# Kernel tuning notes

Measured on AMD Instinct MI355X. Metric: run time of the kernel, lower is better.

The kernel has to match this reference:

```python
import jax, jax.numpy as jnp
import numpy as np

B, C, H, W = 4, 64, 128, 128
NUM_HEAD = 1
SCALE = (C // NUM_HEAD) ** (-0.5)


def setup_inputs():
    key = jax.random.key(0)
    ks = jax.random.split(key, 32)
    def nrm(k, shape, s=0.05):
        return jax.random.normal(k, shape, jnp.float32) * s
    inp = {"x": jax.random.normal(ks[0], (B, C, H, W), jnp.float32)}
    i = 1
    for wn, bn in [("Wq", "bq"), ("Wk", "bk"), ("Wv", "bv"), ("Wl", "bl"), ("Wo", "bo"), ("Wp", "bp")]:
        inp[wn] = nrm(ks[i], (C, C)); i += 1
        inp[bn] = nrm(ks[i], (C,)); i += 1
    inp["sch_dw"] = nrm(ks[i], (C, 1, 5, 1)); i += 1
    inp["sch_dwb"] = nrm(ks[i], (C,)); i += 1
    inp["sch_pw"] = nrm(ks[i], (C, C, 1, 1)); i += 1
    inp["sch_pwb"] = nrm(ks[i], (C,)); i += 1
    inp["scv_dw"] = nrm(ks[i], (C, 1, 1, 5)); i += 1
    inp["scv_dwb"] = nrm(ks[i], (C,)); i += 1
    inp["scv_pw"] = nrm(ks[i], (C, C, 1, 1)); i += 1
    inp["scv_pwb"] = nrm(ks[i], (C,)); i += 1
    inp["convh_w"] = nrm(ks[i], (C, C, 1, 1)); i += 1
    inp["convh_b"] = nrm(ks[i], (C,)); i += 1
    inp["dsc_dw"] = nrm(ks[i], (C, 1, 3, 3)); i += 1
    inp["dsc_dwb"] = nrm(ks[i], (C,)); i += 1
    inp["dsc_pw"] = nrm(ks[i], (C, C, 1, 1)); i += 1
    inp["dsc_pwb"] = nrm(ks[i], (C,)); i += 1
    inp["ln_g"] = jnp.ones((C,), jnp.float32)
    inp["ln_b"] = jnp.zeros((C,), jnp.float32)
    return inp


def _linear(x, w, b):  # x [B,N,C], w [C,C] (torch Linear convention: y = x @ w.T + b)
    return x @ w.T + b


def _dwconv(x, w, b, pad):  # depthwise: x [B,C,H,W], w [C,1,kh,kw]
    y = jax.lax.conv_general_dilated(x, w, (1, 1), [(pad[0], pad[0]), (pad[1], pad[1])],
                                     dimension_numbers=("NCHW", "OIHW", "NCHW"),
                                     feature_group_count=x.shape[1])
    return y + b[None, :, None, None]


def _pwconv(x, w, b):  # 1x1 conv: w [Co,Ci,1,1]
    return jnp.einsum("bchw,oc->bohw", x, w[:, :, 0, 0]) + b[None, :, None, None]


def _attn(q, k, v):  # [B,N,C] each; dense NxN softmax attention
    a = jax.nn.softmax(jnp.einsum("bnc,bmc->bnm", q, k) * SCALE, axis=-1)
    return jnp.einsum("bnm,bmc->bnc", a, v)


def _up2_bilinear(x):  # bilinear, scale 2, align_corners=True
    Bb, Cc, Hh, Ww = x.shape
    def coords(n):
        s = jnp.linspace(0.0, n - 1.0, 2 * n)
        i0 = jnp.floor(s).astype(jnp.int32)
        i1 = jnp.minimum(i0 + 1, n - 1)
        return i0, i1, (s - i0).astype(x.dtype)
    y0, y1, wy = coords(Hh)
    x0, x1, wx = coords(Ww)
    r = x[:, :, y0, :] * (1.0 - wy)[None, None, :, None] + x[:, :, y1, :] * wy[None, None, :, None]
    return r[:, :, :, x0] * (1.0 - wx) + r[:, :, :, x1] * wx


def _forward(x, Wq, bq, Wk, bk, Wv, bv, Wl, bl, Wo, bo, Wp, bp,
             sch_dw, sch_dwb, sch_pw, sch_pwb, scv_dw, scv_dwb, scv_pw, scv_pwb,
             convh_w, convh_b, dsc_dw, dsc_dwb, dsc_pw, dsc_pwb, ln_g, ln_b):
    Bb, Cc, Hh, Ww = x.shape
    # AvgPool2d(2,2)
    xp = x.reshape(Bb, Cc, Hh // 2, 2, Ww // 2, 2).mean((3, 5))
    Hp, Wp_ = Hh // 2, Ww // 2
    N = Hp * Wp_
    # forward_lpg: GAP-gated self-attention producing low-freq prompt
    gap = xp.mean((2, 3), keepdims=True)
    xg = (gap * xp).reshape(Bb, Cc, N).transpose(0, 2, 1)  # [B,N,C]
    q = _linear(xg, Wq, bq); k = _linear(xg, Wk, bk); v = _linear(xg, Wv, bv)
    prompt_l = _linear(_attn(q, k, v), Wl, bl).transpose(0, 2, 1).reshape(Bb, Cc, Hp, Wp_)
    # forward_hpg: separable strip-conv branches -> high-freq prompt
    x_h = _pwconv(jax.nn.gelu(_dwconv(xp, sch_dw, sch_dwb, (2, 0)), approximate=False), sch_pw, sch_pwb)
    x_v = _pwconv(jax.nn.gelu(_dwconv(xp, scv_dw, scv_dwb, (0, 2)), approximate=False), scv_pw, scv_pwb)
    prompt_h = _pwconv(x_h + x_v, convh_w, convh_b)
    # forward_pgc: cross-attention Q=high, K=low, V=linear(x)
    x_V = _linear(xp.reshape(Bb, Cc, N).transpose(0, 2, 1), Wo, bo)
    x_K = prompt_l.reshape(Bb, Cc, N).transpose(0, 2, 1)
    x_Q = prompt_h.reshape(Bb, Cc, N).transpose(0, 2, 1)
    prompt = _attn(x_Q, x_K, x_V)
    prompt = _linear(prompt, Wp, bp) + x_V
    # LayerNorm over channel dim
    mu = prompt.mean(-1, keepdims=True)
    var = jnp.mean((prompt - mu) ** 2, axis=-1, keepdims=True)
    p_norm = (prompt - mu) / jnp.sqrt(var + 1e-5) * ln_g + ln_b
    p_norm = p_norm.transpose(0, 2, 1).reshape(Bb, Cc, Hp, Wp_)
    # dsc: depthwise 3x3 -> GELU -> 1x1, residual
    out = _pwconv(jax.nn.gelu(_dwconv(p_norm, dsc_dw, dsc_dwb, (1, 1)), approximate=False), dsc_pw, dsc_pwb) + p_norm
    return _up2_bilinear(out)


def reference(x, Wq, bq, Wk, bk, Wv, bv, Wl, bl, Wo, bo, Wp, bp,
              sch_dw, sch_dwb, sch_pw, sch_pwb, scv_dw, scv_dwb, scv_pw, scv_pwb,
              convh_w, convh_b, dsc_dw, dsc_dwb, dsc_pw, dsc_pwb, ln_g, ln_b):
    return _forward(x, Wq, bq, Wk, bk, Wv, bv, Wl, bl, Wo, bo, Wp, bp,
                    sch_dw, sch_dwb, sch_pw, sch_pwb, scv_dw, scv_dwb, scv_pw, scv_pwb,
                    convh_w, convh_b, dsc_dw, dsc_dwb, dsc_pw, dsc_pwb, ln_g, ln_b)
```

## Files before the change

### kernel.cpp

```cpp
#include <hip/hip_runtime.h>
#include <math.h>

#define Bn 4
#define Cn 64
#define Np 4096
#define NSPLIT 4
#define SCALE2 0.18033688011112042f

typedef unsigned short ushort_t;
typedef __attribute__((ext_vector_type(4))) float f32x4;
typedef __attribute__((ext_vector_type(8))) short bf16x8;
typedef __attribute__((ext_vector_type(4))) short bf16x4;

__device__ __forceinline__ float gelu_exact(float x) {
    return 0.5f * x * (1.0f + erff(x * 0.70710678118654752440f));
}
__device__ __forceinline__ ushort_t f2bf(float f) {
    unsigned int u = __float_as_uint(f);
    u += 0x7fffu + ((u >> 16) & 1u);
    return (ushort_t)(u >> 16);
}
__device__ __forceinline__ ushort_t f2bf_tr(float f) {
    return (ushort_t)(__float_as_uint(f) >> 16);
}
__device__ __forceinline__ float bf2f(ushort_t h) {
    return __uint_as_float(((unsigned int)h) << 16);
}
__device__ __forceinline__ void gload_lds16(const ushort_t* g, ushort_t* l) {
    __builtin_amdgcn_global_load_lds(
        (const __attribute__((address_space(1))) void*)g,
        (__attribute__((address_space(3))) void*)l, 16, 0, 0);
}
__device__ __forceinline__ bf16x8 cvt8(const float v[8]) {
    bf16x8 r;
    #pragma unroll
    for (int j = 0; j < 8; ++j) r[j] = (short)f2bf(v[j]);
    return r;
}
__device__ __forceinline__ void gemm16b(const bf16x8 af[2], const ushort_t* __restrict__ Wb,
                                        int l16, int quad, f32x4* acc) {
    #pragma unroll
    for (int cb = 0; cb < 4; ++cb) {
        #pragma unroll
        for (int ks = 0; ks < 2; ++ks) {
            bf16x8 bw = *(const bf16x8*)(Wb + (cb * 16 + l16) * 64 + ks * 32 + quad * 8);
            acc[cb] = __builtin_amdgcn_mfma_f32_16x16x32_bf16(af[ks], bw, acc[cb], 0, 0, 0);
        }
    }
}
__device__ __forceinline__ void gemm16Tb(const bf16x8 af[2], const ushort_t* __restrict__ Wb,
                                         int l16, int quad, f32x4* acc) {
    #pragma unroll
    for (int cb = 0; cb < 4; ++cb) {
        #pragma unroll
        for (int ks = 0; ks < 2; ++ks) {
            bf16x8 bw = *(const bf16x8*)(Wb + (cb * 16 + l16) * 64 + ks * 32 + quad * 8);
            acc[cb] = __builtin_amdgcn_mfma_f32_16x16x32_bf16(bw, af[ks], acc[cb], 0, 0, 0);
        }
    }
}
__device__ __forceinline__ void aload(const float* xs, int row, int quad, bf16x8 af[2]) {
    #pragma unroll
    for (int ks = 0; ks < 2; ++ks) {
        float v[8];
        #pragma unroll
        for (int j = 0; j < 8; ++j) v[j] = xs[(ks * 32 + quad * 8 + j) * 65 + row];
        af[ks] = cvt8(v);
    }
}
__device__ __forceinline__ void stage_bchw(const float* __restrict__ X, int b, int n0, int t,
                                           float* xs) {
    #pragma unroll
    for (int u = 0; u < 16; ++u) {
        int idx = t + u * 256;
        int c = idx >> 6, nl = idx & 63;
        xs[c * 65 + nl] = X[((size_t)(b * Cn + c)) * Np + n0 + nl];
    }
}
__device__ __forceinline__ void stage_comb(const ushort_t* __restrict__ OpB, const float* linv,
                                           int b, int n0, int t, float* xs) {
    const size_t SS = (size_t)Bn * Np * Cn;
    int c4 = (t & 15) * 4;
    #pragma unroll
    for (int u = 0; u < 4; ++u) {
        int nl = (t >> 4) + u * 16;
        size_t gi = ((size_t)(b * Np + n0 + nl)) * Cn + c4;
        ushort4 a0 = *(const ushort4*)(OpB + gi);
        ushort4 a1 = *(const ushort4*)(OpB + SS + gi);
        ushort4 a2 = *(const ushort4*)(OpB + 2 * SS + gi);
        ushort4 a3 = *(const ushort4*)(OpB + 3 * SS + gi);
        float li = linv[nl];
        xs[(c4 + 0) * 65 + nl] = (bf2f(a0.x) + bf2f(a1.x) + bf2f(a2.x) + bf2f(a3.x)) * li;
        xs[(c4 + 1) * 65 + nl] = (bf2f(a0.y) + bf2f(a1.y) + bf2f(a2.y) + bf2f(a3.y)) * li;
        xs[(c4 + 2) * 65 + nl] = (bf2f(a0.z) + bf2f(a1.z) + bf2f(a2.z) + bf2f(a3.z)) * li;
        xs[(c4 + 3) * 65 + nl] = (bf2f(a0.w) + bf2f(a1.w) + bf2f(a2.w) + bf2f(a3.w)) * li;
    }
}
__device__ __forceinline__ void store_bnc_T(ushort_t* __restrict__ Y, int b, int n, int quad,
                                            const f32x4* acc, const float* __restrict__ bias,
                                            float mult) {
    #pragma unroll
    for (int cb = 0; cb < 4; ++cb) {
        int o0 = cb * 16 + quad * 4;
        ushort4 pk;
        pk.x = f2bf((acc[cb][0] + bias[o0 + 0]) * mult);
        pk.y = f2bf((acc[cb][1] + bias[o0 + 1]) * mult);
        pk.z = f2bf((acc[cb][2] + bias[o0 + 2]) * mult);
        pk.w = f2bf((acc[cb][3] + bias[o0 + 3]) * mult);
        *(ushort4*)(Y + ((size_t)(b * Np + n)) * Cn + o0) = pk;
    }
}
__device__ __forceinline__ void store_bchw_bf16(ushort_t* __restrict__ Y, int b, int nb, int l16,
                                                const f32x4* acc, const float* __restrict__ bias) {
    #pragma unroll
    for (int cb = 0; cb < 4; ++cb) {
        int col = cb * 16 + l16;
        float bb = bias[col];
        ushort4 pk;
        pk.x = f2bf(acc[cb][0] + bb); pk.y = f2bf(acc[cb][1] + bb);
        pk.z = f2bf(acc[cb][2] + bb); pk.w = f2bf(acc[cb][3] + bb);
        *(ushort4*)(Y + ((size_t)(b * Cn + col)) * Np + nb) = pk;
    }
}

__global__ void avgpool_kernel(const float* __restrict__ x, float* __restrict__ xp,
                               float* __restrict__ gap4k,
                               const float* __restrict__ convh_w, const float* __restrict__ convh_b,
                               const float* __restrict__ sch_pw, const float* __restrict__ sch_pwb,
                               const float* __restrict__ scv_pw, const float* __restrict__ scv_pwb,
                               ushort_t* __restrict__ Wc1b, ushort_t* __restrict__ Wc2b,
                               float* __restrict__ bcv,
                               const float* __restrict__ Wq, const float* __restrict__ Wk,
                               const float* __restrict__ Wv, const float* __restrict__ Wo,
                               const float* __restrict__ Wl, const float* __restrict__ Wp,
                               const float* __restrict__ dscpw, ushort_t* __restrict__ Wball) {
    if (blockIdx.x < 4096) {
        int idx = blockIdx.x * 256 + threadIdx.x;
        int j  = idx & 63;
        int i  = (idx >> 6) & 63;
        int bc = idx >> 12;
        const float* p = x + ((size_t)bc * 128 + 2 * i) * 128 + 2 * j;
        float v = 0.25f * (p[0] + p[1] + p[128] + p[129]);
        xp[idx] = v;
        float s = v;
        #pragma unroll
        for (int off = 1; off < 64; off <<= 1) s += __shfl_xor(s, off, 64);
        __shared__ float sm[4];
        if ((threadIdx.x & 63) == 0) sm[threadIdx.x >> 6] = s;
        __syncthreads();
        if (threadIdx.x == 0) gap4k[blockIdx.x] = sm[0] + sm[1] + sm[2] + sm[3];
    } else if (blockIdx.x < 4128) {
        int g = (blockIdx.x - 4096) * 256 + threadIdx.x;
        int sel = g >> 12, idx = g & 4095;
        int o = idx >> 6, c = idx & 63;
        const float* pw = sel ? scv_pw : sch_pw;
        float acc = 0.f;
        #pragma unroll 8
        for (int m = 0; m < 64; ++m) acc += convh_w[o * 64 + m] * pw[m * 64 + c];
        (sel ? Wc2b : Wc1b)[idx] = f2bf(acc * SCALE2);
        if (g < 64) {
            float ab = convh_b[g];
            for (int m = 0; m < 64; ++m) ab += convh_w[g * 64 + m] * (sch_pwb[m] + scv_pwb[m]);
            bcv[g] = ab * SCALE2;
        }
    } else {
        int g = (blockIdx.x - 4128) * 256 + threadIdx.x;
        int which = g >> 12, idx = g & 4095;
        const float* srcs[7] = {Wq, Wk, Wv, Wo, Wl, Wp, dscpw};
        Wball[g] = f2bf(srcs[which][idx]);
    }
}

__global__ __launch_bounds__(256) void qkv_dw_kernel(
    const float* __restrict__ xp, const float* __restrict__ gap4k,
    const ushort_t* __restrict__ Wqb, const float* __restrict__ bq,
    const ushort_t* __restrict__ Wkb, const float* __restrict__ bk,
    const ushort_t* __restrict__ Wvb, const float* __restrict__ bv,
    const ushort_t* __restrict__ Wob, const float* __restrict__ bo,
    ushort_t* __restrict__ qb, ushort_t* __restrict__ kb, ushort_t* __restrict__ vb,
    float* __restrict__ xV, ushort_t* __restrict__ xVtb,
    const float* __restrict__ wv5, const float* __restrict__ bv5,
    const float* __restrict__ wh5, const float* __restrict__ bh5,
    ushort_t* __restrict__ gh, ushort_t* __restrict__ gv) {
    int b = blockIdx.y, t = threadIdx.x;
    if (blockIdx.x >= 64) {
        int part = blockIdx.x - 64;
        int e = part * 1024 + t * 4;
        size_t base = (size_t)b * (Cn * Np) + e;
        int c = e >> 12, i = (e >> 6) & 63, j = e & 63;
        const float* p = xp + ((size_t)(b * Cn + c)) * Np;
        float accV[4], accH[4];
        #pragma unroll
        for (int k = 0; k < 4; ++k) { accV[k] = bv5[c]; accH[k] = bh5[c]; }
        #pragma unroll
        for (int d = 0; d < 5; ++d) {
            int ii = i + d - 2;
            if (ii >= 0 && ii < 64) {
                f32x4 r = *(const f32x4*)(p + ii * 64 + j);
                float w = wv5[c * 5 + d];
                accV[0] += w * r[0]; accV[1] += w * r[1];
                accV[2] += w * r[2]; accV[3] += w * r[3];
            }
        }
        f32x4 c0 = *(const f32x4*)(p + i * 64 + j);
        float col[8];
        col[2] = c0[0]; col[3] = c0[1]; col[4] = c0[2]; col[5] = c0[3];
        col[0] = (j >= 2)     ? p[i * 64 + j - 2] : 0.f;
        col[1] = (j >= 1)     ? p[i * 64 + j - 1] : 0.f;
        col[6] = (j + 4 < 64) ? p[i * 64 + j + 4] : 0.f;
        col[7] = (j + 5 < 64) ? p[i * 64 + j + 5] : 0.f;
        #pragma unroll
        for (int k = 0; k < 4; ++k) {
            #pragma unroll
            for (int d = 0; d < 5; ++d) accH[k] += wh5[c * 5 + d] * col[k + d];
        }
        ushort4 ph, pv_;
        ph.x = f2bf(gelu_exact(accV[0])); ph.y = f2bf(gelu_exact(accV[1]));
        ph.z = f2bf(gelu_exact(accV[2])); ph.w = f2bf(gelu_exact(accV[3]));
        pv_.x = f2bf(gelu_exact(accH[0])); pv_.y = f2bf(gelu_exact(accH[1]));
        pv_.z = f2bf(gelu_exact(accH[2])); pv_.w = f2bf(gelu_exact(accH[3]));
        *(ushort4*)(gh + base) = ph;
        *(ushort4*)(gv + base) = pv_;
        return;
    }
    __shared__ float xs[64 * 65];
    __shared__ float gl[64];
    int n0 = blockIdx.x * 64;
    int wv_ = t >> 6, lane = t & 63, l16 = lane & 15, quad = lane >> 4;
    stage_bchw(xp, b, n0, t, xs);
    if (t < 64) {
        float s = 0.f;
        #pragma unroll
        for (int u = 0; u < 16; ++u) s += gap4k[(b * 64 + t) * 16 + u];
        gl[t] = s * (1.f / 4096.f);
    }
    __syncthreads();
    int row = wv_ * 16 + l16;
    int n   = n0 + wv_ * 16 + l16;
    int nb  = n0 + wv_ * 16 + quad * 4;
    bf16x8 ar[2], ag[2];
    #pragma unroll
    for (int ks = 0; ks < 2; ++ks) {
        float vr[8], vg[8];
        #pragma unroll
        for (int j = 0; j < 8; ++j) {
            int k = ks * 32 + quad * 8 + j;
            float xv = xs[k * 65 + row];
            vr[j] = xv; vg[j] = xv * gl[k];
        }
        ar[ks] = cvt8(vr); ag[ks] = cvt8(vg);
    }
    f32x4 acc[4];
    #pragma unroll
    for (int cb = 0; cb < 4; ++cb) acc[cb] = (f32x4){0.f, 0.f, 0.f, 0.f};
    gemm16Tb(ag, Wqb, l16, quad, acc);
    store_bnc_T(qb, b, n, quad, acc, bq, SCALE2);
    #pragma unroll
    for (int cb = 0; cb < 4; ++cb) acc[cb] = (f32x4){0.f, 0.f, 0.f, 0.f};
    gemm16Tb(ag, Wkb, l16, quad, acc);
    store_bnc_T(kb, b, n, quad, acc, bk, 1.f);
    #pragma unroll
    for (int cb = 0; cb < 4; ++cb) acc[cb] = (f32x4){0.f, 0.f, 0.f, 0.f};
    gemm16b(ag, Wvb, l16, quad, acc);
    store_bchw_bf16(vb, b, nb, l16, acc, bv);
    #pragma unroll
    for (int cb = 0; cb < 4; ++cb) acc[cb] = (f32x4){0.f, 0.f, 0.f, 0.f};
    gemm16b(ar, Wob, l16, quad, acc);
    #pragma unroll
    for (int cb = 0; cb < 4; ++cb) {
        int col = cb * 16 + l16;
        float bb = bo[col];
        ushort4 pk;
        float y0 = acc[cb][0] + bb, y1 = acc[cb][1] + bb, y2 = acc[cb][2] + bb, y3 = acc[cb][3] + bb;
        xV[((size_t)(b * Np + nb + 0)) * Cn + col] = y0;
        xV[((size_t)(b * Np + nb + 1)) * Cn + col] = y1;
        xV[((size_t)(b * Np + nb + 2)) * Cn + col] = y2;
        xV[((size_t)(b * Np + nb + 3)) * Cn + col] = y3;
        pk.x = f2bf(y0); pk.y = f2bf(y1); pk.z = f2bf(y2); pk.w = f2bf(y3);
        *(ushort4*)(xVtb + ((size_t)(b * Cn + col)) * Np + nb) = pk;
    }
}

__device__ __forceinline__ void attn_wave(
    int wid, int b, const ushort_t* __restrict__ Qb, const ushort_t* __restrict__ Kb,
    const ushort_t* __restrict__ Vtb, ushort_t* __restrict__ OpB, float* __restrict__ Lpart,
    ushort_t* lds ) {
    int split = wid >> 7;
    int qt    = wid & 127;
    int n0    = qt * 32;
    int lane  = threadIdx.x & 63;
    int l16   = lane & 15, quad = lane >> 4;
    int kvbase = split * (Np / NSPLIT);

    const ushort_t* qp = Qb + ((size_t)(b * Np) + n0 + l16) * Cn + quad * 8;
    bf16x8 aq00 = *(const bf16x8*)(qp);
    bf16x8 aq01 = *(const bf16x8*)(qp + 32);
    bf16x8 aq10 = *(const bf16x8*)(qp + 16 * Cn);
    bf16x8 aq11 = *(const bf16x8*)(qp + 16 * Cn + 32);
    asm volatile("s_waitcnt vmcnt(0)" ::: "memory");

    f32x4 oa0[4], oa1[4];
    float psum0 = 0.f, psum1 = 0.f;
    #pragma unroll
    for (int db = 0; db < 4; ++db) {
        oa0[db] = (f32x4){0.f, 0.f, 0.f, 0.f};
        oa1[db] = (f32x4){0.f, 0.f, 0.f, 0.f};
    }

    const ushort_t* gK = Kb + ((size_t)b * Np + kvbase + (lane >> 3)) * Cn
                            + (((lane & 7) ^ (lane >> 3)) * 8);
    const ushort_t* gV = Vtb + ((size_t)(b * Cn) + (lane >> 1)) * Np + kvbase + (lane & 1) * 8;
    ushort_t* kl = lds;
    ushort_t* vl = lds + 2048;

    const ushort_t* kr0 = lds + l16 * 64 + ((quad      ^ (l16 & 7))) * 8;
    const ushort_t* kr1 = lds + l16 * 64 + (((quad + 4) ^ (l16 & 7))) * 8;
    const ushort_t* vrb = lds + 2048 + l16 * 16 + quad * 4;

    auto stage = [&](int buf) {
        ushort_t* kd = kl + buf * 1024;
        gload_lds16(gK,       kd);
        gload_lds16(gK + 512, kd + 512);
        ushort_t* vd = vl + buf * 1024;
        gload_lds16(gV,                   vd);
        gload_lds16(gV + (size_t)32 * Np, vd + 512);
        gK += 16 * Cn;
        gV += 16;
    };

    auto compute = [&](int ko) {
        bf16x8 k0 = *(const bf16x8*)(kr0 + ko);
        bf16x8 k1 = *(const bf16x8*)(kr1 + ko);
        f32x4 sa0 = (f32x4){0.f, 0.f, 0.f, 0.f};
        f32x4 sa1 = (f32x4){0.f, 0.f, 0.f, 0.f};
        __builtin_amdgcn_s_setprio(1);
        sa0 = __builtin_amdgcn_mfma_f32_16x16x32_bf16(k0, aq00, sa0, 0, 0, 0);
        sa0 = __builtin_amdgcn_mfma_f32_16x16x32_bf16(k1, aq01, sa0, 0, 0, 0);
        sa1 = __builtin_amdgcn_mfma_f32_16x16x32_bf16(k0, aq10, sa1, 0, 0, 0);
        sa1 = __builtin_amdgcn_mfma_f32_16x16x32_bf16(k1, aq11, sa1, 0, 0, 0);
        __builtin_amdgcn_s_setprio(0);
        float p0 = exp2f(sa0[0]), p1 = exp2f(sa0[1]), p2 = exp2f(sa0[2]), p3 = exp2f(sa0[3]);
        psum0 += (p0 + p1) + (p2 + p3);
        bf16x4 pb0;
        pb0[0] = (short)f2bf_tr(p0); pb0[1] = (short)f2bf_tr(p1);
        pb0[2] = (short)f2bf_tr(p2); pb0[3] = (short)f2bf_tr(p3);
        float q0 = exp2f(sa1[0]), q1 = exp2f(sa1[1]), q2 = exp2f(sa1[2]), q3 = exp2f(sa1[3]);
        psum1 += (q0 + q1) + (q2 + q3);
        bf16x4 pb1;
        pb1[0] = (short)f2bf_tr(q0); pb1[1] = (short)f2bf_tr(q1);
        pb1[2] = (short)f2bf_tr(q2); pb1[3] = (short)f2bf_tr(q3);
        __builtin_amdgcn_s_setprio(1);
        #pragma unroll
        for (int db = 0; db < 4; ++db) {
            bf16x4 av = *(const bf16x4*)(vrb + ko + db * 256);
            oa0[db] = __builtin_amdgcn_mfma_f32_16x16x16bf16_1k(av, pb0, oa0[db], 0, 0, 0);
            oa1[db] = __builtin_amdgcn_mfma_f32_16x16x16bf16_1k(av, pb1, oa1[db], 0, 0, 0);
        }
        __builtin_amdgcn_s_setprio(0);
    };

    const int NT = (Np / NSPLIT) / 16;
    stage(0);
    #pragma unroll 1
    for (int mm = 0; mm < NT / 2; ++mm) {
        stage(1);
        asm volatile("s_waitcnt vmcnt(4)" ::: "memory");
        compute(0);
        if (mm < NT / 2 - 1) {
            stage(0);
            asm volatile("s_waitcnt vmcnt(4)" ::: "memory");
        } else {
            asm volatile("s_waitcnt vmcnt(0)" ::: "memory");
        }
        compute(1024);
    }

    psum0 += __shfl_xor(psum0, 16, 64);
    psum0 += __shfl_xor(psum0, 32, 64);
    psum1 += __shfl_xor(psum1, 16, 64);
    psum1 += __shfl_xor(psum1, 32, 64);
    size_t obase = ((size_t)(split * Bn + b)) * Np;
    int n = n0 + l16;
    if (quad == 0) {
        Lpart[obase + n]      = psum0;
        Lpart[obase + n + 16] = psum1;
    }
    #pragma unroll
    for (int db = 0; db < 4; ++db) {
        ushort4 pk;
        pk.x = f2bf(oa0[db][0]); pk.y = f2bf(oa0[db][1]);
        pk.z = f2bf(oa0[db][2]); pk.w = f2bf(oa0[db][3]);
        *(ushort4*)(OpB + (obase + n) * Cn + db * 16 + quad * 4) = pk;
        ushort4 qk;
        qk.x = f2bf(oa1[db][0]); qk.y = f2bf(oa1[db][1]);
        qk.z = f2bf(oa1[db][2]); qk.w = f2bf(oa1[db][3]);
        *(ushort4*)(OpB + (obase + n + 16) * Cn + db * 16 + quad * 4) = qk;
    }
}

__device__ __forceinline__ void hpg_body(
    int tile, int b, const ushort_t* __restrict__ gh, const ushort_t* __restrict__ gv,
    const ushort_t* __restrict__ Wc1b, const ushort_t* __restrict__ Wc2b,
    const float* __restrict__ bcv,
    ushort_t* __restrict__ xQb, ushort_t* smem) {
    ushort_t* xs1 = smem;
    ushort_t* xs2 = smem + 4608;
    int n0 = tile * 64, t = threadIdx.x;
    int wv_ = t >> 6, lane = t & 63, l16 = lane & 15, quad = lane >> 4;
    #pragma unroll
    for (int u = 0; u < 4; ++u) {
        int lin = u * 256 + t;
        int c = lin >> 4, nl4 = (lin & 15) * 4;
        size_t gi = ((size_t)(b * Cn + c)) * Np + n0 + nl4;
        ushort4 g1 = *(const ushort4*)(gh + gi);
        ushort4 g2 = *(const ushort4*)(gv + gi);
        xs1[(nl4 + 0) * 72 + c] = g1.x; xs1[(nl4 + 1) * 72 + c] = g1.y;
        xs1[(nl4 + 2) * 72 + c] = g1.z; xs1[(nl4 + 3) * 72 + c] = g1.w;
        xs2[(nl4 + 0) * 72 + c] = g2.x; xs2[(nl4 + 1) * 72 + c] = g2.y;
        xs2[(nl4 + 2) * 72 + c] = g2.z; xs2[(nl4 + 3) * 72 + c] = g2.w;
    }
    __syncthreads();
    int row = wv_ * 16 + l16;
    bf16x8 a1[2], a2[2];
    #pragma unroll
    for (int ks = 0; ks < 2; ++ks) {
        a1[ks] = *(const bf16x8*)(xs1 + row * 72 + ks * 32 + quad * 8);
        a2[ks] = *(const bf16x8*)(xs2 + row * 72 + ks * 32 + quad * 8);
    }
    f32x4 acc[4];
    #pragma unroll
    for (int cb = 0; cb < 4; ++cb) acc[cb] = (f32x4){0.f, 0.f, 0.f, 0.f};
    gemm16Tb(a1, Wc1b, l16, quad, acc);
    gemm16Tb(a2, Wc2b, l16, quad, acc);
    store_bnc_T(xQb, b, n0 + wv_ * 16 + l16, quad, acc, bcv, 1.f);
}

__global__ __launch_bounds__(256) void attn_hpg_kernel(
    const ushort_t* __restrict__ Qb, const ushort_t* __restrict__ Kb,
    const ushort_t* __restrict__ Vtb, ushort_t* __restrict__ OpB, float* __restrict__ Lpart,
    const ushort_t* __restrict__ gh, const ushort_t* __restrict__ gv,
    const ushort_t* __restrict__ Wc1b, const ushort_t* __restrict__ Wc2b,
    const float* __restrict__ bcv, ushort_t* __restrict__ xQb) {
    __shared__ ushort_t smem[16384];
    int b = blockIdx.y;
    if (blockIdx.x < 128) {
        int wave = threadIdx.x >> 6;
        attn_wave(blockIdx.x * 4 + wave, b, Qb, Kb, Vtb, OpB, Lpart, smem + wave * 4096);
    } else {
        hpg_body(blockIdx.x - 128, b, gh, gv, Wc1b, Wc2b, bcv, xQb, smem);
    }
}

__global__ __launch_bounds__(256) void wl_mfma(
    const ushort_t* __restrict__ OpB, const float* __restrict__ Lp,
    const ushort_t* __restrict__ Wlb, const float* __restrict__ bl, ushort_t* __restrict__ xKb) {
    __shared__ float xs[64 * 65];
    __shared__ float linv[64];
    int b = blockIdx.y, n0 = blockIdx.x * 64, t = threadIdx.x;
    int wv_ = t >> 6, lane = t & 63, l16 = lane & 15, quad = lane >> 4;
    if (t < 64) {
        size_t li = (size_t)b * Np + n0 + t;
        const size_t LS = (size_t)Bn * Np;
        linv[t] = 1.f / (Lp[li] + Lp[LS + li] + Lp[2 * LS + li] + Lp[3 * LS + li]);
    }
    __syncthreads();
    stage_comb(OpB, linv, b, n0, t, xs);
    __syncthreads();
    bf16x8 af[2];
    aload(xs, wv_ * 16 + l16, quad, af);
    f32x4 acc[4];
    #pragma unroll
    for (int cb = 0; cb < 4; ++cb) acc[cb] = (f32x4){0.f, 0.f, 0.f, 0.f};
    gemm16Tb(af, Wlb, l16, quad, acc);
    store_bnc_T(xKb, b, n0 + wv_ * 16 + l16, quad, acc, bl, 1.f);
}

__global__ __launch_bounds__(256) void linln_mfma(
    const ushort_t* __restrict__ OpB, const float* __restrict__ Lp,
    const ushort_t* __restrict__ Wpb, const float* __restrict__ bp,
    const float* __restrict__ xV, const float* __restrict__ g, const float* __restrict__ beta,
    float* __restrict__ out) {
    __shared__ float xs[64 * 65];
    __shared__ float linv[64];
    int b = blockIdx.y, n0 = blockIdx.x * 64, t = threadIdx.x;
    int wv_ = t >> 6, lane = t & 63, l16 = lane & 15, quad = lane >> 4;
    if (t < 64) {
        size_t li = (size_t)b * Np + n0 + t;
        const size_t LS = (size_t)Bn * Np;
        linv[t] = 1.f / (Lp[li] + Lp[LS + li] + Lp[2 * LS + li] + Lp[3 * LS + li]);
    }
    __syncthreads();
    stage_comb(OpB, linv, b, n0, t, xs);
    __syncthreads();
    bf16x8 af[2];
    aload(xs, wv_ * 16 + l16, quad, af);
    f32x4 acc[4];
    #pragma unroll
    for (int cb = 0; cb < 4; ++cb) acc[cb] = (f32x4){0.f, 0.f, 0.f, 0.f};
    gemm16b(af, Wpb, l16, quad, acc);
    int nb = n0 + wv_ * 16 + quad * 4;
    float vals[4][4], gc[4], bec[4];
    #pragma unroll
    for (int cb = 0; cb < 4; ++cb) {
        int col = cb * 16 + l16;
        float bb = bp[col];
        gc[cb] = g[col]; bec[cb] = beta[col];
        #pragma unroll
        for (int r = 0; r < 4; ++r)
            vals[cb][r] = acc[cb][r] + bb + xV[((size_t)(b * Np + nb + r)) * Cn + col];
    }
    f32x4 yn[4];
    #pragma unroll
    for (int r = 0; r < 4; ++r) {
        float s = 0.f, s2 = 0.f;
        #pragma unroll
        for (int cb = 0; cb < 4; ++cb) { s += vals[cb][r]; s2 += vals[cb][r] * vals[cb][r]; }
        #pragma unroll
        for (int off = 1; off < 16; off <<= 1) {
            s  += __shfl_xor(s, off, 64);
            s2 += __shfl_xor(s2, off, 64);
        }
        float mu  = s * (1.f / 64.f);
        float var = s2 * (1.f / 64.f) - mu * mu;
        float ivs = rsqrtf(var + 1e-5f);
        #pragma unroll
        for (int cb = 0; cb < 4; ++cb)
            yn[cb][r] = (vals[cb][r] - mu) * ivs * gc[cb] + bec[cb];
    }
    #pragma unroll
    for (int cb = 0; cb < 4; ++cb)
        *(f32x4*)(out + ((size_t)(b * Cn + cb * 16 + l16)) * Np + nb) = yn[cb];
}

__global__ __launch_bounds__(256) void dsc_mfma(
    const float* __restrict__ X, const float* __restrict__ dw, const float* __restrict__ dwb,
    const ushort_t* __restrict__ Wb, const float* __restrict__ bias, float* __restrict__ out) {
    __shared__ float xs[64 * 65];
    int b = blockIdx.y, irow = blockIdx.x, n0 = irow * 64, t = threadIdx.x;
    int wv_ = t >> 6, lane = t & 63, l16 = lane & 15, quad = lane >> 4;
    int j = t & 63;
    #pragma unroll
    for (int u = 0; u < 16; ++u) {
        int c = (t >> 6) + u * 4;
        const float* p = X + ((size_t)(b * Cn + c)) * Np + n0;
        float acc = dwb[c];
        #pragma unroll
        for (int dy = 0; dy < 3; ++dy) {
            int ii = irow + dy - 1;
            if (ii < 0 || ii >= 64) continue;
            const float* pr = p + (dy - 1) * 64;
            #pragma unroll
            for (int dx = 0; dx < 3; ++dx) {
                int jj = j + dx - 1;
                if (jj < 0 || jj >= 64) continue;
                acc += dw[c * 9 + dy * 3 + dx] * pr[jj];
            }
        }
        xs[c * 65 + j] = gelu_exact(acc);
    }
    __syncthreads();
    bf16x8 af[2];
    aload(xs, wv_ * 16 + l16, quad, af);
    f32x4 acc[4];
    #pragma unroll
    for (int cb = 0; cb < 4; ++cb) acc[cb] = (f32x4){0.f, 0.f, 0.f, 0.f};
    gemm16b(af, Wb, l16, quad, acc);
    int nb = n0 + wv_ * 16 + quad * 4;
    #pragma unroll
    for (int cb = 0; cb < 4; ++cb) {
        int col = cb * 16 + l16;
        float bb = bias[col];
        size_t oi = ((size_t)(b * Cn + col)) * Np + nb;
        f32x4 rv = *(const f32x4*)(X + oi);
        f32x4 v4;
        #pragma unroll
        for (int r = 0; r < 4; ++r) v4[r] = acc[cb][r] + bb + rv[r];
        *(f32x4*)(out + oi) = v4;
    }
}

__global__ void upsample_kernel(const float* __restrict__ in, float* __restrict__ out) {
    int idx = blockIdx.x * 256 + threadIdx.x;
    int x4 = (idx & 31) * 4;
    int y  = (idx >> 5) & 127;
    int bc = idx >> 12;
    float sy = y * (63.f / 127.f);
    int y0 = (int)sy;
    float fy = sy - y0;
    int y1 = min(y0 + 1, 63);
    const float* p0 = in + (size_t)bc * Np + y0 * 64;
    const float* p1 = in + (size_t)bc * Np + y1 * 64;
    f32x4 o;
    #pragma unroll
    for (int k = 0; k < 4; ++k) {
        int xo = x4 + k;
        float sx = xo * (63.f / 127.f);
        int x0 = (int)sx;
        float fx = sx - x0;
        int x1 = min(x0 + 1, 63);
        float r0 = p0[x0] + (p0[x1] - p0[x0]) * fx;
        float r1 = p1[x0] + (p1[x1] - p1[x0]) * fx;
        o[k] = r0 + (r1 - r0) * fy;
    }
    *(f32x4*)(out + (size_t)idx * 4) = o;
}

extern "C" void kernel_launch(void* const* d_in, const int* in_sizes, int n_in,
                              void* d_out, int out_size, void* d_ws, size_t ws_size,
                              hipStream_t stream) {
    const float* x       = (const float*)d_in[0];
    const float* Wq      = (const float*)d_in[1];
    const float* bq      = (const float*)d_in[2];
    const float* Wk      = (const float*)d_in[3];
    const float* bk      = (const float*)d_in[4];
    const float* Wv      = (const float*)d_in[5];
    const float* bv      = (const float*)d_in[6];
    const float* Wl      = (const float*)d_in[7];
    const float* bl      = (const float*)d_in[8];
    const float* Wo      = (const float*)d_in[9];
    const float* bo      = (const float*)d_in[10];
    const float* Wp      = (const float*)d_in[11];
    const float* bp      = (const float*)d_in[12];
    const float* sch_dw  = (const float*)d_in[13];
    const float* sch_dwb = (const float*)d_in[14];
    const float* sch_pw  = (const float*)d_in[15];
    const float* sch_pwb = (const float*)d_in[16];
    const float* scv_dw  = (const float*)d_in[17];
    const float* scv_dwb = (const float*)d_in[18];
    const float* scv_pw  = (const float*)d_in[19];
    const float* scv_pwb = (const float*)d_in[20];
    const float* convh_w = (const float*)d_in[21];
    const float* convh_b = (const float*)d_in[22];
    const float* dsc_dw  = (const float*)d_in[23];
    const float* dsc_dwb = (const float*)d_in[24];
    const float* dsc_pw  = (const float*)d_in[25];
    const float* dsc_pwb = (const float*)d_in[26];
    const float* ln_g    = (const float*)d_in[27];
    const float* ln_b    = (const float*)d_in[28];

    float* ws = (float*)d_ws;
    const size_t SZ = (size_t)Bn * Np * Cn;
    float* xp   = ws;
    float* xV   = ws + SZ;
    ushort_t* ghb = (ushort_t*)(ws + 2 * SZ);
    ushort_t* gh  = ghb;
    ushort_t* gv  = ghb + SZ;
    float* f2   = ws + 2 * SZ;
    ushort_t* bws  = (ushort_t*)(ws + 3 * SZ);
    ushort_t* qb   = bws;
    ushort_t* kb_  = bws + SZ;
    ushort_t* vb   = bws + 2 * SZ;
    ushort_t* xKb  = bws + 3 * SZ;
    ushort_t* xVtb = bws + 4 * SZ;
    ushort_t* xQb  = bws + 5 * SZ;
    ushort_t* OpB  = (ushort_t*)(ws + 6 * SZ);
    float* gap4k  = ws + 8 * SZ;
    float* Lpart  = gap4k + 4096;
    float* wcslot = Lpart + (size_t)NSPLIT * Bn * Np;
    ushort_t* Wc1b = (ushort_t*)wcslot;
    ushort_t* Wc2b = Wc1b + 4096;
    float* bcv  = wcslot + 4096;
    ushort_t* Wball = (ushort_t*)(bcv + 64);
    ushort_t* Wqb   = Wball;
    ushort_t* Wkb   = Wball + 4096;
    ushort_t* Wvb   = Wball + 8192;
    ushort_t* Wob   = Wball + 12288;
    ushort_t* Wlb   = Wball + 16384;
    ushort_t* Wpb   = Wball + 20480;
    ushort_t* Wdscb = Wball + 24576;

    dim3 g64(64, Bn);

    avgpool_kernel<<<4096 + 32 + 112, 256, 0, stream>>>(x, xp, gap4k,
                                                  convh_w, convh_b, sch_pw, sch_pwb,
                                                  scv_pw, scv_pwb, Wc1b, Wc2b, bcv,
                                                  Wq, Wk, Wv, Wo, Wl, Wp, dsc_pw, Wball);
    qkv_dw_kernel<<<dim3(64 + 256, Bn), 256, 0, stream>>>(
        xp, gap4k, Wqb, bq, Wkb, bk, Wvb, bv, Wob, bo,
        qb, kb_, vb, xV, xVtb, sch_dw, sch_dwb, scv_dw, scv_dwb, gh, gv);
    attn_hpg_kernel<<<dim3(128 + 64, Bn), 256, 0, stream>>>(
        qb, kb_, vb, OpB, Lpart, gh, gv, Wc1b, Wc2b, bcv, xQb);
    wl_mfma<<<g64, 256, 0, stream>>>(OpB, Lpart, Wlb, bl, xKb);
    attn_hpg_kernel<<<dim3(128, Bn), 256, 0, stream>>>(
        xQb, xKb, xVtb, OpB, Lpart, gh, gv, Wc1b, Wc2b, bcv, xQb);
    linln_mfma<<<g64, 256, 0, stream>>>(OpB, Lpart, Wpb, bp, xV, ln_g, ln_b, xp);
    dsc_mfma<<<g64, 256, 0, stream>>>(xp, dsc_dw, dsc_dwb, Wdscb, dsc_pwb, f2);
    upsample_kernel<<<4096, 256, 0, stream>>>(f2, (float*)d_out);
}
```

Baseline: 267.0 us.

## Double KV split count in attention and swizzle V tile in LDS

Raises the flash-attention KV split factor from 4 to 8, doubling the attention grid to 1024 blocks so more of the GPU's compute units are occupied. The combine step in the Wl and LN kernels now loops over all partials, and the workspace layout is shifted to make room for the larger partial-output buffer. Separately, the V tile's LDS layout gets an XOR swizzle on its 8-element halves to reduce bank conflicts on reads. The cost is twice the partial-output traffic written and then reduced by the combine kernels.

```diff
diff --git a/kernel.cpp b/kernel.cpp
--- a/kernel.cpp
+++ b/kernel.cpp
@@ -4,7 +4,7 @@
 #define Bn 4
 #define Cn 64
 #define Np 4096
-#define NSPLIT 4
+#define NSPLIT 8
 #define SCALE2 0.18033688011112042f
 
 typedef unsigned short ushort_t;
@@ -85,15 +85,17 @@
     for (int u = 0; u < 4; ++u) {
         int nl = (t >> 4) + u * 16;
         size_t gi = ((size_t)(b * Np + n0 + nl)) * Cn + c4;
-        ushort4 a0 = *(const ushort4*)(OpB + gi);
-        ushort4 a1 = *(const ushort4*)(OpB + SS + gi);
-        ushort4 a2 = *(const ushort4*)(OpB + 2 * SS + gi);
-        ushort4 a3 = *(const ushort4*)(OpB + 3 * SS + gi);
+        float s0 = 0.f, s1 = 0.f, s2 = 0.f, s3 = 0.f;
+        #pragma unroll
+        for (int sp = 0; sp < NSPLIT; ++sp) {
+            ushort4 a = *(const ushort4*)(OpB + (size_t)sp * SS + gi);
+            s0 += bf2f(a.x); s1 += bf2f(a.y); s2 += bf2f(a.z); s3 += bf2f(a.w);
+        }
         float li = linv[nl];
-        xs[(c4 + 0) * 65 + nl] = (bf2f(a0.x) + bf2f(a1.x) + bf2f(a2.x) + bf2f(a3.x)) * li;
-        xs[(c4 + 1) * 65 + nl] = (bf2f(a0.y) + bf2f(a1.y) + bf2f(a2.y) + bf2f(a3.y)) * li;
-        xs[(c4 + 2) * 65 + nl] = (bf2f(a0.z) + bf2f(a1.z) + bf2f(a2.z) + bf2f(a3.z)) * li;
-        xs[(c4 + 3) * 65 + nl] = (bf2f(a0.w) + bf2f(a1.w) + bf2f(a2.w) + bf2f(a3.w)) * li;
+        xs[(c4 + 0) * 65 + nl] = s0 * li;
+        xs[(c4 + 1) * 65 + nl] = s1 * li;
+        xs[(c4 + 2) * 65 + nl] = s2 * li;
+        xs[(c4 + 3) * 65 + nl] = s3 * li;
     }
 }
 __device__ __forceinline__ void store_bnc_T(ushort_t* __restrict__ Y, int b, int n, int quad,
@@ -309,13 +311,15 @@
 
     const ushort_t* gK = Kb + ((size_t)b * Np + kvbase + (lane >> 3)) * Cn
                             + (((lane & 7) ^ (lane >> 3)) * 8);
-    const ushort_t* gV = Vtb + ((size_t)(b * Cn) + (lane >> 1)) * Np + kvbase + (lane & 1) * 8;
+    const ushort_t* gV = Vtb + ((size_t)(b * Cn) + (lane >> 1)) * Np + kvbase
+                             + (((lane & 1) ^ ((lane >> 3) & 1)) * 8);
     ushort_t* kl = lds;
     ushort_t* vl = lds + 2048;
 
     const ushort_t* kr0 = lds + l16 * 64 + ((quad      ^ (l16 & 7))) * 8;
     const ushort_t* kr1 = lds + l16 * 64 + (((quad + 4) ^ (l16 & 7))) * 8;
-    const ushort_t* vrb = lds + 2048 + l16 * 16 + quad * 4;
+    const ushort_t* vrb = lds + 2048 + l16 * 16
+                        + (((quad >> 1) ^ ((l16 >> 2) & 1)) * 8) + (quad & 1) * 4;
 
     auto stage = [&](int buf) {
         ushort_t* kd = kl + buf * 1024;
@@ -443,11 +447,11 @@
     const float* __restrict__ bcv, ushort_t* __restrict__ xQb) {
     __shared__ ushort_t smem[16384];
     int b = blockIdx.y;
-    if (blockIdx.x < 128) {
+    if (blockIdx.x < 256) {
         int wave = threadIdx.x >> 6;
         attn_wave(blockIdx.x * 4 + wave, b, Qb, Kb, Vtb, OpB, Lpart, smem + wave * 4096);
     } else {
-        hpg_body(blockIdx.x - 128, b, gh, gv, Wc1b, Wc2b, bcv, xQb, smem);
+        hpg_body(blockIdx.x - 256, b, gh, gv, Wc1b, Wc2b, bcv, xQb, smem);
     }
 }
 
@@ -461,7 +465,10 @@
     if (t < 64) {
         size_t li = (size_t)b * Np + n0 + t;
         const size_t LS = (size_t)Bn * Np;
-        linv[t] = 1.f / (Lp[li] + Lp[LS + li] + Lp[2 * LS + li] + Lp[3 * LS + li]);
+        float s = 0.f;
+        #pragma unroll
+        for (int sp = 0; sp < NSPLIT; ++sp) s += Lp[(size_t)sp * LS + li];
+        linv[t] = 1.f / s;
     }
     __syncthreads();
     stage_comb(OpB, linv, b, n0, t, xs);
@@ -487,7 +494,10 @@
     if (t < 64) {
         size_t li = (size_t)b * Np + n0 + t;
         const size_t LS = (size_t)Bn * Np;
-        linv[t] = 1.f / (Lp[li] + Lp[LS + li] + Lp[2 * LS + li] + Lp[3 * LS + li]);
+        float s = 0.f;
+        #pragma unroll
+        for (int sp = 0; sp < NSPLIT; ++sp) s += Lp[(size_t)sp * LS + li];
+        linv[t] = 1.f / s;
     }
     __syncthreads();
     stage_comb(OpB, linv, b, n0, t, xs);
@@ -654,7 +664,7 @@
     ushort_t* xVtb = bws + 4 * SZ;
     ushort_t* xQb  = bws + 5 * SZ;
     ushort_t* OpB  = (ushort_t*)(ws + 6 * SZ);
-    float* gap4k  = ws + 8 * SZ;
+    float* gap4k  = ws + 10 * SZ;
     float* Lpart  = gap4k + 4096;
     float* wcslot = Lpart + (size_t)NSPLIT * Bn * Np;
     ushort_t* Wc1b = (ushort_t*)wcslot;
@@ -678,10 +688,10 @@
     qkv_dw_kernel<<<dim3(64 + 256, Bn), 256, 0, stream>>>(
         xp, gap4k, Wqb, bq, Wkb, bk, Wvb, bv, Wob, bo,
         qb, kb_, vb, xV, xVtb, sch_dw, sch_dwb, scv_dw, scv_dwb, gh, gv);
-    attn_hpg_kernel<<<dim3(128 + 64, Bn), 256, 0, stream>>>(
+    attn_hpg_kernel<<<dim3(256 + 64, Bn), 256, 0, stream>>>(
         qb, kb_, vb, OpB, Lpart, gh, gv, Wc1b, Wc2b, bcv, xQb);
     wl_mfma<<<g64, 256, 0, stream>>>(OpB, Lpart, Wlb, bl, xKb);
-    attn_hpg_kernel<<<dim3(128, Bn), 256, 0, stream>>>(
+    attn_hpg_kernel<<<dim3(256, Bn), 256, 0, stream>>>(
         xQb, xKb, xVtb, OpB, Lpart, gh, gv, Wc1b, Wc2b, bcv, xQb);
     linln_mfma<<<g64, 256, 0, stream>>>(OpB, Lpart, Wpb, bp, xV, ln_g, ln_b, xp);
     dsc_mfma<<<g64, 256, 0, stream>>>(xp, dsc_dw, dsc_dwb, Wdscb, dsc_pwb, f2);
```

New measurement: 262.7 us. Within noise of the previous version (-1.6%).
